# Performance work log

Hardware: AMD Instinct MI355X
Metric: run time of the kernel (lower is better)

The kernel has to match this reference:

```python
import jax, jax.numpy as jnp
import numpy as np

N_HEAD = 32
N_KV_HEAD = 8
HEAD_DIM = 64
ROPE_BASE = 10000.0


def _rope_cos_sin(T, dtype):
    # inv_freq over even dims; freqs: [T, HEAD_DIM//2]
    inv_freq = 1.0 / (ROPE_BASE ** (jnp.arange(0, HEAD_DIM, 2, dtype=jnp.float32) / HEAD_DIM))
    freqs = jnp.arange(T, dtype=jnp.float32)[:, None] * inv_freq[None, :]
    return jnp.cos(freqs).astype(dtype), jnp.sin(freqs).astype(dtype)


def _apply_rope(x, cos, sin):
    # x: [B, H, T, D]; cos/sin: [T, D//2]. Original chunks cat(freqs,freqs) so
    # cos1==cos2==cos(freqs), sin1==sin2==sin(freqs) -> standard rotate-half.
    x1, x2 = jnp.split(x, 2, axis=-1)
    c = cos[None, None]
    s = sin[None, None]
    return jnp.concatenate([x1 * c - x2 * s, x1 * s + x2 * c], axis=-1)


def setup_inputs() -> dict:
    key = jax.random.key(0)
    ks = jax.random.split(key, 5)
    B, T, C = 2, 2048, 2048
    kv_dim = N_KV_HEAD * HEAD_DIM
    sc = 1.0 / np.sqrt(C)
    return {
        "x": jax.random.normal(ks[0], (B, T, C), jnp.float32),
        "Wq": jax.random.normal(ks[1], (C, C), jnp.float32) * sc,
        "Wk": jax.random.normal(ks[2], (C, kv_dim), jnp.float32) * sc,
        "Wv": jax.random.normal(ks[3], (C, kv_dim), jnp.float32) * sc,
        "Wo": jax.random.normal(ks[4], (C, C), jnp.float32) * sc,
    }


def reference(x, Wq, Wk, Wv, Wo):
    B, T, C = x.shape
    n_rep = N_HEAD // N_KV_HEAD
    # projections -> [B, H, T, D]
    q = (x @ Wq).reshape(B, T, N_HEAD, HEAD_DIM).transpose(0, 2, 1, 3)
    k = (x @ Wk).reshape(B, T, N_KV_HEAD, HEAD_DIM).transpose(0, 2, 1, 3)
    v = (x @ Wv).reshape(B, T, N_KV_HEAD, HEAD_DIM).transpose(0, 2, 1, 3)
    cos, sin = _rope_cos_sin(T, x.dtype)
    q = _apply_rope(q, cos, sin)
    k = _apply_rope(k, cos, sin)
    # GQA: q head h attends kv head h // n_rep (repeat_interleave semantics).
    # Group q as [B, KV, n_rep, T, D] and broadcast k/v instead of materializing.
    qg = q.reshape(B, N_KV_HEAD, n_rep, T, HEAD_DIM)
    scale = 1.0 / np.sqrt(HEAD_DIM)
    scores = jnp.einsum("bgrqd,bgkd->bgrqk", qg, k) * scale  # [B,KV,rep,T,T]
    causal = jnp.tril(jnp.ones((T, T), dtype=bool))
    scores = jnp.where(causal[None, None, None], scores, -jnp.inf)
    att = jax.nn.softmax(scores, axis=-1)
    y = jnp.einsum("bgrqk,bgkd->bgrqd", att, v)  # [B,KV,rep,T,D]
    y = y.reshape(B, N_HEAD, T, HEAD_DIM).transpose(0, 2, 1, 3).reshape(B, T, C)
    return y @ Wo
```

## Files before the change

### kernel.cpp

```cpp
#include <hip/hip_runtime.h>
#include <hip/hip_bf16.h>


typedef __hip_bfloat16 bf16_t;
typedef __bf16 bf16x8 __attribute__((ext_vector_type(8)));
typedef float f32x4 __attribute__((ext_vector_type(4)));

#define AS1 __attribute__((address_space(1)))
#define AS3 __attribute__((address_space(3)))

__device__ __forceinline__ void gload_lds16(const void* g, void* l) {
  __builtin_amdgcn_global_load_lds((const AS1 unsigned int*)g,
                                   (AS3 unsigned int*)l, 16, 0, 0);
}

__device__ __forceinline__ float fast_exp2(float x) {
#if __has_builtin(__builtin_amdgcn_exp2f)
  return __builtin_amdgcn_exp2f(x);
#else
  return exp2f(x);
#endif
}

__device__ __forceinline__ unsigned int pack_bf16_rnd(unsigned int u0, unsigned int u1) {
  u0 += 0x8000u; u1 += 0x8000u;
#if __has_builtin(__builtin_amdgcn_perm)
  return __builtin_amdgcn_perm(u1, u0, 0x07060302u);
#else
  return (u1 & 0xffff0000u) | (u0 >> 16);
#endif
}

__device__ __forceinline__ void store_out(float* p, float v) { *p = v; }
__device__ __forceinline__ void store_out(bf16_t* p, float v) { *p = __float2bfloat16(v); }

__global__ void prep(const float* __restrict__ x, const float* __restrict__ Wq,
                     const float* __restrict__ Wk, const float* __restrict__ Wv,
                     const float* __restrict__ Wo, bf16_t* __restrict__ xb,
                     bf16_t* __restrict__ wqkvt, bf16_t* __restrict__ wot) {
  const int bid = blockIdx.x, tid = threadIdx.x;
  if (bid < 2048) {
#pragma unroll
    for (int k = 0; k < 4; ++k) {
      int i = bid * 1024 + k * 256 + tid;
      float4 v = ((const float4*)x)[i];
      bf16_t o[4] = {__float2bfloat16(v.x), __float2bfloat16(v.y),
                     __float2bfloat16(v.z), __float2bfloat16(v.w)};
      ((ushort4*)xb)[i] = *(ushort4*)o;
    }
    return;
  }
  const float* W; bf16_t* dst; int ncols, bx, by;
  if (bid < 6144)       { int l = bid - 2048;  W = Wq; dst = wqkvt;               ncols = 2048; bx = l & 63; by = l >> 6; }
  else if (bid < 10240) { int l = bid - 6144;  W = Wo; dst = wot;                 ncols = 2048; bx = l & 63; by = l >> 6; }
  else if (bid < 11264) { int l = bid - 10240; W = Wk; dst = wqkvt + 2048L * 2048; ncols = 512; bx = l & 15; by = l >> 4; }
  else                  { int l = bid - 11264; W = Wv; dst = wqkvt + 2560L * 2048; ncols = 512; bx = l & 15; by = l >> 4; }
  __shared__ float tile[32][33];
  const int tx = tid & 31, ty = tid >> 5;
  const int n0 = bx * 32, k0 = by * 32;
#pragma unroll
  for (int i = 0; i < 4; ++i)
    tile[ty + 8 * i][tx] = W[(long)(k0 + ty + 8 * i) * ncols + n0 + tx];
  __syncthreads();
#pragma unroll
  for (int i = 0; i < 4; ++i)
    dst[(long)(n0 + ty + 8 * i) * 2048 + k0 + tx] = __float2bfloat16(tile[tx][ty + 8 * i]);
}

__global__ void rope_vt(bf16_t* __restrict__ qkv, bf16_t* __restrict__ vt) {
  const int bid = blockIdx.x, tid = threadIdx.x;
  __shared__ bf16_t tile[32][33];
  if (bid < 2560) {
    int i = bid * 256 + tid;
    int oct = i & 3;
    int rem = i >> 2;
    int hp = rem % 40;
    int row = rem / 40;
    int t = row & 2047;
    int colbase = (hp < 32) ? (hp * 64) : (2048 + (hp - 32) * 64);
    long base = (long)row * 3072 + colbase + oct * 8;
    bf16x8 x1 = *(bf16x8*)(qkv + base);
    bf16x8 x2 = *(bf16x8*)(qkv + base + 32);
    float sc = (hp < 32) ? 0.18033688011112043f : 1.0f;
    bf16x8 o1, o2;
#pragma unroll
    for (int jj = 0; jj < 8; ++jj) {
      int d = oct * 8 + jj;
      float inv_freq = exp2f(-(float)d * 0.4152410118074032f);
      float ang = (float)t * inv_freq;
      float rev = ang * 0.15915494309189535f;
      float fr = (rev - rintf(rev)) * 6.283185307179586f;
      float sv = __sinf(fr), cv = __cosf(fr);
      float a = __bfloat162float(((const __hip_bfloat16*)&x1)[jj]);
      float b = __bfloat162float(((const __hip_bfloat16*)&x2)[jj]);
      ((__hip_bfloat16*)&o1)[jj] = __float2bfloat16((a * cv - b * sv) * sc);
      ((__hip_bfloat16*)&o2)[jj] = __float2bfloat16((a * sv + b * cv) * sc);
    }
    *(bf16x8*)(qkv + base) = o1;
    *(bf16x8*)(qkv + base + 32) = o2;
    return;
  }
  int l = bid - 2560;
  int t0 = (l & 63) * 32;
  int rest = l >> 6;
  int d0 = (rest & 1) * 32;
  int bk = rest >> 1;
  int bb = bk >> 3, kv = bk & 7;
  const int tx = tid & 31, ty = tid >> 5;
  const bf16_t* src = qkv + (long)(bb * 2048) * 3072 + 2560 + kv * 64;
#pragma unroll
  for (int i = 0; i < 4; ++i)
    tile[ty + 8 * i][tx] = src[(long)(t0 + ty + 8 * i) * 3072 + d0 + tx];
  __syncthreads();
#pragma unroll
  for (int i = 0; i < 4; ++i)
    vt[((long)bk * 64 + d0 + ty + 8 * i) * 2048 + t0 + tx] = tile[tx][ty + 8 * i];
}

template <typename OutT>
__global__ __launch_bounds__(256, 3)
void gemm_bt(const bf16_t* __restrict__ A, const bf16_t* __restrict__ Bt,
             OutT* __restrict__ C, int M, int N, int K) {
  __shared__ __align__(16) bf16_t As[128 * 64];
  __shared__ __align__(16) bf16_t Bs[128 * 64];
  const int tid = threadIdx.x;
  const int wave = tid >> 6, lane = tid & 63, g = lane >> 4, l15 = lane & 15;
  const int m0 = blockIdx.y * 128, n0 = blockIdx.x * 128;
  const int mw = (wave >> 1) * 64, nw = (wave & 1) * 64;
  const bf16_t* Ab = A + (long)m0 * K;
  const bf16_t* Bb = Bt + (long)n0 * K;
  f32x4 acc[4][4] = {};
  const int nkt = K >> 6;
  for (int kt = 0; kt < nkt; ++kt) {
    __syncthreads();
#pragma unroll
    for (int i = 0; i < 4; ++i) {
      int c = i * 256 + tid;
      int row = c >> 3, pos = c & 7;
      int gcol = ((pos ^ (row & 7)) * 8);
      gload_lds16(Ab + (long)row * K + kt * 64 + gcol, &As[c * 8]);
      gload_lds16(Bb + (long)row * K + kt * 64 + gcol, &Bs[c * 8]);
    }
    __syncthreads();
#pragma unroll
    for (int ks = 0; ks < 2; ++ks) {
      bf16x8 af[4], bq[4];
#pragma unroll
      for (int i = 0; i < 4; ++i) {
        int pos = ((ks * 4 + g) ^ (l15 & 7)) * 8;
        af[i] = *(const bf16x8*)&As[(mw + i * 16 + l15) * 64 + pos];
        bq[i] = *(const bf16x8*)&Bs[(nw + i * 16 + l15) * 64 + pos];
      }
#pragma unroll
      for (int i = 0; i < 4; ++i)
#pragma unroll
        for (int j = 0; j < 4; ++j)
          acc[i][j] = __builtin_amdgcn_mfma_f32_16x16x32_bf16(af[i], bq[j], acc[i][j], 0, 0, 0);
    }
  }
#pragma unroll
  for (int i = 0; i < 4; ++i)
#pragma unroll
    for (int j = 0; j < 4; ++j) {
      int r = m0 + mw + i * 16 + g * 4;
      int cn = n0 + nw + j * 16 + l15;
#pragma unroll
      for (int ii = 0; ii < 4; ++ii)
        store_out(&C[(long)(r + ii) * N + cn], acc[i][j][ii]);
    }
}

__global__ __launch_bounds__(256, 4)
void flash_attn(const bf16_t* __restrict__ qkv, const bf16_t* __restrict__ vt,
                bf16_t* __restrict__ y) {
  constexpr int T = 2048, LDQ = 3072;
  __shared__ __align__(16) bf16_t Ks[2][64 * 64];
  __shared__ __align__(16) bf16_t Vs[2][64 * 64];
  __shared__ __align__(16) bf16_t Ps[4][1024];
  const int tid = threadIdx.x, wave = tid >> 6, lane = tid & 63, g = lane >> 4, l15 = lane & 15;
  const int j = blockIdx.x;
  const int h = blockIdx.y, b = blockIdx.z;
  const int qt0 = (j < 8) ? (15 - j) : (j - 8);
  const int qt = ((h >> 4) & 1) ? (15 - qt0) : qt0;
  const int kvh = h >> 2;
  const bf16_t* qbase = qkv + (long)(b * T + qt * 128) * LDQ + h * 64;
  const bf16_t* kbase = qkv + (long)(b * T) * LDQ + 2048 + kvh * 64;
  const bf16_t* vbase = vt + (long)((b * 8 + kvh) * 64) * T;

  bf16x8 qf[2][2];
#pragma unroll
  for (int ms = 0; ms < 2; ++ms)
#pragma unroll
    for (int hh = 0; hh < 2; ++hh)
      qf[ms][hh] = *(const bf16x8*)(qbase + (long)(wave * 32 + ms * 16 + l15) * LDQ + hh * 32 + g * 8);

  bf16x8 onef;
#pragma unroll
  for (int i = 0; i < 8; ++i) onef[i] = (__bf16)1.0f;

  f32x4 o[2][4] = {};
  f32x4 lacc[2] = {};
  bf16_t* Pw = &Ps[wave][0];
  const int sw = (l15 >> 1) & 3;
  const f32x4 fz = {0.f, 0.f, 0.f, 0.f};

  auto stage = [&](int kt, int buf) {
#pragma unroll
    for (int i = 0; i < 2; ++i) {
      int c = i * 256 + tid;
      int row = c >> 3, pos = c & 7;
      gload_lds16(kbase + (long)(kt * 64 + row) * LDQ + ((pos ^ (row & 7)) * 8),
                  &Ks[buf][c * 8]);
      gload_lds16(vbase + (long)row * T + kt * 64 + ((pos ^ (row & 7)) * 8),
                  &Vs[buf][c * 8]);
    }
  };

  stage(0, 0);
  const int nkt = 2 * qt + 2;
  for (int kt = 0; kt < nkt; ++kt) {
    __syncthreads();
    if (kt + 1 < nkt) stage(kt + 1, (kt + 1) & 1);
    const bf16_t* Kc = Ks[kt & 1];
    const bf16_t* Vc = Vs[kt & 1];
    const int dk = kt - 2 * qt;
    const bool diag = (dk >= 0);

#pragma unroll
    for (int ks = 0; ks < 2; ++ks) {
      f32x4 s[2][2];
#pragma unroll
      for (int nsl = 0; nsl < 2; ++nsl) {
        int krow = ks * 32 + nsl * 16 + l15;
        bf16x8 kf0 = *(const bf16x8*)&Kc[krow * 64 + ((g ^ (l15 & 7)) * 8)];
        bf16x8 kf1 = *(const bf16x8*)&Kc[krow * 64 + (((4 + g) ^ (l15 & 7)) * 8)];
#pragma unroll
        for (int ms = 0; ms < 2; ++ms) {
          f32x4 t = __builtin_amdgcn_mfma_f32_16x16x32_bf16(kf0, qf[ms][0], fz, 0, 0, 0);
          s[ms][nsl] = __builtin_amdgcn_mfma_f32_16x16x32_bf16(kf1, qf[ms][1], t, 0, 0, 0);
        }
      }
      bf16x8 pf[2];
#pragma unroll
      for (int ms = 0; ms < 2; ++ms) {
#pragma unroll
        for (int nsl = 0; nsl < 2; ++nsl) {
          unsigned int u[4];
#pragma unroll
          for (int ii = 0; ii < 4; ++ii) {
            float p = fast_exp2(s[ms][nsl][ii]);
            if (diag && (dk * 64 + ks * 32 + nsl * 16 + g * 4 + ii >
                         wave * 32 + ms * 16 + l15)) p = 0.f;
            u[ii] = __builtin_bit_cast(unsigned int, p);
          }
          uint2 dw;
          dw.x = pack_bf16_rnd(u[0], u[1]);
          dw.y = pack_bf16_rnd(u[2], u[3]);
          int pp = (nsl * 2 + (g >> 1)) ^ sw;
          *(uint2*)&Pw[(ms * 16 + l15) * 32 + pp * 8 + (g & 1) * 4] = dw;
        }
        pf[ms] = *(const bf16x8*)&Pw[(ms * 16 + l15) * 32 + ((g ^ sw) * 8)];
        lacc[ms] = __builtin_amdgcn_mfma_f32_16x16x32_bf16(pf[ms], onef, lacc[ms], 0, 0, 0);
      }
#pragma unroll
      for (int ds = 0; ds < 4; ++ds) {
        bf16x8 vf = *(const bf16x8*)&Vc[(ds * 16 + l15) * 64 + (((ks * 4 + g) ^ (l15 & 7)) * 8)];
        o[0][ds] = __builtin_amdgcn_mfma_f32_16x16x32_bf16(pf[0], vf, o[0][ds], 0, 0, 0);
        o[1][ds] = __builtin_amdgcn_mfma_f32_16x16x32_bf16(pf[1], vf, o[1][ds], 0, 0, 0);
      }
    }
  }

  __syncthreads();
  bf16_t* E = (bf16_t*)&Vs[0][0] + wave * 1152;
#pragma unroll
  for (int ms = 0; ms < 2; ++ms) {
    f32x4 linv;
#pragma unroll
    for (int ii = 0; ii < 4; ++ii) linv[ii] = 1.0f / lacc[ms][ii];
#pragma unroll
    for (int ds = 0; ds < 4; ++ds)
#pragma unroll
      for (int ii = 0; ii < 4; ++ii)
        E[(g * 4 + ii) * 72 + ds * 16 + l15] = __float2bfloat16(o[ms][ds][ii] * linv[ii]);
    bf16x8 r0 = *(const bf16x8*)&E[l15 * 72 + g * 16];
    bf16x8 r1 = *(const bf16x8*)&E[l15 * 72 + g * 16 + 8];
    int q = qt * 128 + wave * 32 + ms * 16 + l15;
    *(bf16x8*)&y[(long)(b * T + q) * 2048 + h * 64 + g * 16] = r0;
    *(bf16x8*)&y[(long)(b * T + q) * 2048 + h * 64 + g * 16 + 8] = r1;
  }
}

extern "C" void kernel_launch(void* const* d_in, const int* in_sizes, int n_in,
                              void* d_out, int out_size, void* d_ws, size_t ws_size,
                              hipStream_t stream) {
  const float* x  = (const float*)d_in[0];
  const float* Wq = (const float*)d_in[1];
  const float* Wk = (const float*)d_in[2];
  const float* Wv = (const float*)d_in[3];
  const float* Wo = (const float*)d_in[4];
  float* out = (float*)d_out;
  char* ws = (char*)d_ws;

  bf16_t* xb    = (bf16_t*)(ws);
  bf16_t* wqkvt = (bf16_t*)(ws + 16777216);
  bf16_t* wot   = (bf16_t*)(ws + 16777216 + 12582912);
  bf16_t* qkvb  = (bf16_t*)(ws + 16777216 + 12582912 + 8388608);
  bf16_t* vtb   = (bf16_t*)(ws + 16777216 + 12582912 + 8388608 + 25165824);
  bf16_t* yb = xb;

  prep<<<12288, 256, 0, stream>>>(x, Wq, Wk, Wv, Wo, xb, wqkvt, wot);
  gemm_bt<bf16_t><<<dim3(24, 32), 256, 0, stream>>>(xb, wqkvt, qkvb, 4096, 3072, 2048);
  rope_vt<<<4608, 256, 0, stream>>>(qkvb, vtb);
  flash_attn<<<dim3(16, 32, 2), 256, 0, stream>>>(qkvb, vtb, yb);
  gemm_bt<float><<<dim3(16, 32), 256, 0, stream>>>(yb, wot, out, 4096, 2048, 2048);
}
```

Baseline: 279.4 us.

## Fuse RoPE and V transpose into QKV GEMM epilogue; tweak attention scheduling

Removes the separate rope_vt kernel. RoPE rotation and the query scale are now applied in the QKV GEMM epilogue, and V is written directly in transposed layout from the accumulators. This saves one launch and a full read/write pass over the QKV buffer. The flash attention kernel also precomputes its staging pointers and raises wave priority around the MFMA sections with s_setprio. In exchange, the GEMM epilogue does extra sin/cos work, and the transposed V stores are narrower and less coalesced.

Result: faster. 266.4 us (-4.7%).

```diff
diff --git a/kernel.cpp b/kernel.cpp
--- a/kernel.cpp
+++ b/kernel.cpp
@@ -67,60 +67,10 @@
     dst[(long)(n0 + ty + 8 * i) * 2048 + k0 + tx] = __float2bfloat16(tile[tx][ty + 8 * i]);
 }
 
-__global__ void rope_vt(bf16_t* __restrict__ qkv, bf16_t* __restrict__ vt) {
-  const int bid = blockIdx.x, tid = threadIdx.x;
-  __shared__ bf16_t tile[32][33];
-  if (bid < 2560) {
-    int i = bid * 256 + tid;
-    int oct = i & 3;
-    int rem = i >> 2;
-    int hp = rem % 40;
-    int row = rem / 40;
-    int t = row & 2047;
-    int colbase = (hp < 32) ? (hp * 64) : (2048 + (hp - 32) * 64);
-    long base = (long)row * 3072 + colbase + oct * 8;
-    bf16x8 x1 = *(bf16x8*)(qkv + base);
-    bf16x8 x2 = *(bf16x8*)(qkv + base + 32);
-    float sc = (hp < 32) ? 0.18033688011112043f : 1.0f;
-    bf16x8 o1, o2;
-#pragma unroll
-    for (int jj = 0; jj < 8; ++jj) {
-      int d = oct * 8 + jj;
-      float inv_freq = exp2f(-(float)d * 0.4152410118074032f);
-      float ang = (float)t * inv_freq;
-      float rev = ang * 0.15915494309189535f;
-      float fr = (rev - rintf(rev)) * 6.283185307179586f;
-      float sv = __sinf(fr), cv = __cosf(fr);
-      float a = __bfloat162float(((const __hip_bfloat16*)&x1)[jj]);
-      float b = __bfloat162float(((const __hip_bfloat16*)&x2)[jj]);
-      ((__hip_bfloat16*)&o1)[jj] = __float2bfloat16((a * cv - b * sv) * sc);
-      ((__hip_bfloat16*)&o2)[jj] = __float2bfloat16((a * sv + b * cv) * sc);
-    }
-    *(bf16x8*)(qkv + base) = o1;
-    *(bf16x8*)(qkv + base + 32) = o2;
-    return;
-  }
-  int l = bid - 2560;
-  int t0 = (l & 63) * 32;
-  int rest = l >> 6;
-  int d0 = (rest & 1) * 32;
-  int bk = rest >> 1;
-  int bb = bk >> 3, kv = bk & 7;
-  const int tx = tid & 31, ty = tid >> 5;
-  const bf16_t* src = qkv + (long)(bb * 2048) * 3072 + 2560 + kv * 64;
-#pragma unroll
-  for (int i = 0; i < 4; ++i)
-    tile[ty + 8 * i][tx] = src[(long)(t0 + ty + 8 * i) * 3072 + d0 + tx];
-  __syncthreads();
-#pragma unroll
-  for (int i = 0; i < 4; ++i)
-    vt[((long)bk * 64 + d0 + ty + 8 * i) * 2048 + t0 + tx] = tile[tx][ty + 8 * i];
-}
-
-template <typename OutT>
+template <typename OutT, int MODE>
 __global__ __launch_bounds__(256, 3)
 void gemm_bt(const bf16_t* __restrict__ A, const bf16_t* __restrict__ Bt,
-             OutT* __restrict__ C, int M, int N, int K) {
+             OutT* __restrict__ C, int M, int N, int K, bf16_t* __restrict__ vt) {
   __shared__ __align__(16) bf16_t As[128 * 64];
   __shared__ __align__(16) bf16_t Bs[128 * 64];
   const int tid = threadIdx.x;
@@ -158,16 +108,60 @@
           acc[i][j] = __builtin_amdgcn_mfma_f32_16x16x32_bf16(af[i], bq[j], acc[i][j], 0, 0, 0);
     }
   }
-#pragma unroll
-  for (int i = 0; i < 4; ++i)
-#pragma unroll
-    for (int j = 0; j < 4; ++j) {
-      int r = m0 + mw + i * 16 + g * 4;
-      int cn = n0 + nw + j * 16 + l15;
-#pragma unroll
-      for (int ii = 0; ii < 4; ++ii)
-        store_out(&C[(long)(r + ii) * N + cn], acc[i][j][ii]);
-    }
+
+  if (MODE == 1) {
+    const int cnb = n0 + nw;
+    if (cnb >= 2560) {
+      const int kv = (cnb - 2560) >> 6;
+      const int bb = m0 >> 11;
+#pragma unroll
+      for (int i = 0; i < 4; ++i) {
+        const int t0 = (m0 & 2047) + mw + i * 16 + g * 4;
+#pragma unroll
+        for (int j = 0; j < 4; ++j) {
+          const int d = j * 16 + l15;
+          bf16_t o4[4];
+#pragma unroll
+          for (int ii = 0; ii < 4; ++ii) o4[ii] = __float2bfloat16(acc[i][j][ii]);
+          *(ushort4*)&vt[((long)((bb * 8 + kv) * 64 + d)) * 2048 + t0] = *(ushort4*)o4;
+        }
+      }
+    } else {
+      const float sc = (cnb < 2048) ? 0.18033688011112043f : 1.0f;
+#pragma unroll
+      for (int jp = 0; jp < 2; ++jp) {
+        const int d = jp * 16 + l15;
+        const float invf = exp2f(-(float)d * 0.4152410118074032f);
+        const int cn = cnb + jp * 16 + l15;
+#pragma unroll
+        for (int i = 0; i < 4; ++i) {
+          const int r0 = m0 + mw + i * 16 + g * 4;
+#pragma unroll
+          for (int ii = 0; ii < 4; ++ii) {
+            const int t = (r0 + ii) & 2047;
+            float ang = (float)t * invf;
+            float rev = ang * 0.15915494309189535f;
+            float fr = (rev - rintf(rev)) * 6.283185307179586f;
+            float sv = __sinf(fr), cv = __cosf(fr);
+            float x1 = acc[i][jp][ii], x2 = acc[i][jp + 2][ii];
+            store_out(&C[(long)(r0 + ii) * N + cn],      (x1 * cv - x2 * sv) * sc);
+            store_out(&C[(long)(r0 + ii) * N + cn + 32], (x1 * sv + x2 * cv) * sc);
+          }
+        }
+      }
+    }
+  } else {
+#pragma unroll
+    for (int i = 0; i < 4; ++i)
+#pragma unroll
+      for (int j = 0; j < 4; ++j) {
+        int r = m0 + mw + i * 16 + g * 4;
+        int cn = n0 + nw + j * 16 + l15;
+#pragma unroll
+        for (int ii = 0; ii < 4; ++ii)
+          store_out(&C[(long)(r + ii) * N + cn], acc[i][j][ii]);
+      }
+  }
 }
 
 __global__ __launch_bounds__(256, 4)
@@ -204,23 +198,29 @@
   const int sw = (l15 >> 1) & 3;
   const f32x4 fz = {0.f, 0.f, 0.f, 0.f};
 
-  auto stage = [&](int kt, int buf) {
-#pragma unroll
-    for (int i = 0; i < 2; ++i) {
-      int c = i * 256 + tid;
-      int row = c >> 3, pos = c & 7;
-      gload_lds16(kbase + (long)(kt * 64 + row) * LDQ + ((pos ^ (row & 7)) * 8),
-                  &Ks[buf][c * 8]);
-      gload_lds16(vbase + (long)row * T + kt * 64 + ((pos ^ (row & 7)) * 8),
-                  &Vs[buf][c * 8]);
-    }
+  const int c0 = tid, c1 = 256 + tid;
+  const int row0 = c0 >> 3, pos0 = c0 & 7, sw0 = ((pos0 ^ (row0 & 7)) * 8);
+  const int row1 = c1 >> 3, pos1 = c1 & 7, sw1 = ((pos1 ^ (row1 & 7)) * 8);
+  const bf16_t* kp0 = kbase + (long)row0 * LDQ + sw0;
+  const bf16_t* kp1 = kbase + (long)row1 * LDQ + sw1;
+  const bf16_t* vp0 = vbase + (long)row0 * T + sw0;
+  const bf16_t* vp1 = vbase + (long)row1 * T + sw1;
+  const int l0 = c0 * 8, l1 = c1 * 8;
+
+  auto stage = [&](int buf) {
+    gload_lds16(kp0, &Ks[buf][l0]);
+    gload_lds16(vp0, &Vs[buf][l0]);
+    gload_lds16(kp1, &Ks[buf][l1]);
+    gload_lds16(vp1, &Vs[buf][l1]);
+    kp0 += 64 * LDQ; kp1 += 64 * LDQ;
+    vp0 += 64;       vp1 += 64;
   };
 
-  stage(0, 0);
+  stage(0);
   const int nkt = 2 * qt + 2;
   for (int kt = 0; kt < nkt; ++kt) {
     __syncthreads();
-    if (kt + 1 < nkt) stage(kt + 1, (kt + 1) & 1);
+    if (kt + 1 < nkt) stage((kt + 1) & 1);
     const bf16_t* Kc = Ks[kt & 1];
     const bf16_t* Vc = Vs[kt & 1];
     const int dk = kt - 2 * qt;
@@ -229,6 +229,7 @@
 #pragma unroll
     for (int ks = 0; ks < 2; ++ks) {
       f32x4 s[2][2];
+      __builtin_amdgcn_s_setprio(1);
 #pragma unroll
       for (int nsl = 0; nsl < 2; ++nsl) {
         int krow = ks * 32 + nsl * 16 + l15;
@@ -240,6 +241,7 @@
           s[ms][nsl] = __builtin_amdgcn_mfma_f32_16x16x32_bf16(kf1, qf[ms][1], t, 0, 0, 0);
         }
       }
+      __builtin_amdgcn_s_setprio(0);
       bf16x8 pf[2];
 #pragma unroll
       for (int ms = 0; ms < 2; ++ms) {
@@ -262,12 +264,14 @@
         pf[ms] = *(const bf16x8*)&Pw[(ms * 16 + l15) * 32 + ((g ^ sw) * 8)];
         lacc[ms] = __builtin_amdgcn_mfma_f32_16x16x32_bf16(pf[ms], onef, lacc[ms], 0, 0, 0);
       }
+      __builtin_amdgcn_s_setprio(1);
 #pragma unroll
       for (int ds = 0; ds < 4; ++ds) {
         bf16x8 vf = *(const bf16x8*)&Vc[(ds * 16 + l15) * 64 + (((ks * 4 + g) ^ (l15 & 7)) * 8)];
         o[0][ds] = __builtin_amdgcn_mfma_f32_16x16x32_bf16(pf[0], vf, o[0][ds], 0, 0, 0);
         o[1][ds] = __builtin_amdgcn_mfma_f32_16x16x32_bf16(pf[1], vf, o[1][ds], 0, 0, 0);
       }
+      __builtin_amdgcn_s_setprio(0);
     }
   }
 
@@ -310,8 +314,7 @@
   bf16_t* yb = xb;
 
   prep<<<12288, 256, 0, stream>>>(x, Wq, Wk, Wv, Wo, xb, wqkvt, wot);
-  gemm_bt<bf16_t><<<dim3(24, 32), 256, 0, stream>>>(xb, wqkvt, qkvb, 4096, 3072, 2048);
-  rope_vt<<<4608, 256, 0, stream>>>(qkvb, vtb);
+  gemm_bt<bf16_t, 1><<<dim3(24, 32), 256, 0, stream>>>(xb, wqkvt, qkvb, 4096, 3072, 2048, vtb);
   flash_attn<<<dim3(16, 32, 2), 256, 0, stream>>>(qkvb, vtb, yb);
-  gemm_bt<float><<<dim3(16, 32), 256, 0, stream>>>(yb, wot, out, 4096, 2048, 2048);
-}
+  gemm_bt<float, 0><<<dim3(16, 32), 256, 0, stream>>>(yb, wot, out, 4096, 2048, 2048, nullptr);
+}
```
